# Optimization experiments

Measured on AMD Instinct MI355X. Metric: run time of the kernel, lower is better.

The kernel has to match this reference:

```python
import jax, jax.numpy as jnp
import numpy as np

B, S, D_IN, D_OUT = 2, 2048, 4096, 4096
E, K, R = 8, 2, 16
SCALING = 32.0 / 16.0  # lora_alpha / r (use_rslora=False)


def setup_inputs() -> dict:
    key = jax.random.key(0)
    ks = jax.random.split(key, 6)
    x = jax.random.normal(ks[0], (B, S, D_IN), dtype=jnp.float32)
    gate_w = jax.random.normal(ks[1], (E, D_IN), dtype=jnp.float32) * 0.02
    base_w = jax.random.normal(ks[2], (D_OUT, D_IN), dtype=jnp.float32) * 0.02
    base_b = jax.random.normal(ks[3], (D_OUT,), dtype=jnp.float32) * 0.02
    lora_A = jax.random.normal(ks[4], (E, R, D_IN), dtype=jnp.float32) * 0.02
    lora_B = jax.random.normal(ks[5], (E, D_OUT, R), dtype=jnp.float32) * 0.02
    return {"x": x, "gate_w": gate_w, "base_w": base_w, "base_b": base_b,
            "lora_A": lora_A, "lora_B": lora_B}


def reference(x, gate_w, base_w, base_b, lora_A, lora_B):
    # gate + top-k routing
    gate_logits = jnp.einsum('bsd,ed->bse', x, gate_w)           # [B,S,E]
    weights, selected = jax.lax.top_k(gate_logits, K)            # [B,S,K]
    weights = jax.nn.softmax(weights.astype(jnp.float32), axis=2).astype(x.dtype)
    # base linear
    result = jnp.einsum('bsd,od->bso', x, base_w) + base_b       # [B,S,O]
    # scatter routing weights into a dense per-expert weight map [B,S,E]
    w_full = jnp.sum(jax.nn.one_hot(selected, E, dtype=x.dtype) * weights[..., None], axis=2)
    # low-rank LoRA for every expert (tiny r), combine weighted per token
    low = jnp.einsum('bsd,erd->ebsr', x, lora_A)                 # [E,B,S,R]
    lora_out = jnp.einsum('ebsr,eor,bse->bso', low, lora_B, w_full)
    result = result + SCALING * lora_out
    return result
```

## Files before the change

kernel.cpp:

```cpp
#include <hip/hip_runtime.h>
#include <hip/hip_bf16.h>

typedef unsigned short u16;
typedef __bf16  bf16x8 __attribute__((ext_vector_type(8)));
typedef float   f32x4  __attribute__((ext_vector_type(4)));

#define T_TOK 4096
#define DIN   4096
#define DOUT  4096
#define NEXP  8
#define ER    128
#define SPLIT 8
#define KCH   (DIN / SPLIT)

#define OFF_XB    0u
#define OFF_WB    33554432u
#define OFF_AB    67108864u
#define OFF_BS2   68157440u
#define OFF_U     69206016u
#define OFF_BBF   70254592u
#define OFF_LG    70270976u
#define OFF_GPART 70402048u

__device__ __forceinline__ void async16(void* lds, const void* g) {
    __builtin_amdgcn_global_load_lds(
        (const __attribute__((address_space(1))) void*)g,
        (__attribute__((address_space(3))) void*)lds,
        16, 0, 0);
}

static __device__ __forceinline__ u16 f2b(float f) {
    __hip_bfloat16 h = __float2bfloat16(f);
    return *(u16*)&h;
}

__device__ __forceinline__ bf16x8 lds8(const u16* base, int row, int grp) {
    return *(const bf16x8*)((const char*)base + row * 128 + (((grp ^ row) & 7) * 16));
}

__global__ __launch_bounds__(256) void convert_big(const float* __restrict__ x,
                                                   const float* __restrict__ w,
                                                   uint4* __restrict__ xb,
                                                   uint4* __restrict__ wb) {
    int gid = blockIdx.x * 256 + threadIdx.x;
    const float4* s = (const float4*)((gid < 2097152) ? x : w);
    uint4* dst      = (gid < 2097152) ? xb : wb;
    int li = gid & 2097151;
    float4 a = s[2 * li], b = s[2 * li + 1];
    uint4 o;
    o.x = (unsigned)f2b(a.x) | ((unsigned)f2b(a.y) << 16);
    o.y = (unsigned)f2b(a.z) | ((unsigned)f2b(a.w) << 16);
    o.z = (unsigned)f2b(b.x) | ((unsigned)f2b(b.y) << 16);
    o.w = (unsigned)f2b(b.z) | ((unsigned)f2b(b.w) << 16);
    dst[li] = o;
}

__global__ __launch_bounds__(256) void pack_small(const float* __restrict__ lora_A,
                                                  const float* __restrict__ lora_B,
                                                  const float* __restrict__ base_b,
                                                  u16* __restrict__ ab,
                                                  u16* __restrict__ bs2,
                                                  float* __restrict__ bbf) {
    int idx = blockIdx.x * 256 + threadIdx.x;
    if (idx < 524288) {
        ab[idx] = f2b(lora_A[idx]);
    } else if (idx < 1048576) {
        int j = idx - 524288;
        int o = j >> 7, c = j & 127, e = c >> 4, r = c & 15;
        bs2[j] = f2b(lora_B[(e * DOUT + o) * 16 + r] * 2.0f);
    } else if (idx < 1052672) {
        int j = idx - 1048576;
        bbf[j] = base_b[j];
    }
}

__global__ __launch_bounds__(256) void gate_logits(const float* __restrict__ x,
                                                   const float* __restrict__ gw,
                                                   float* __restrict__ Lg) {
    const int w = threadIdx.x >> 6, lid = threadIdx.x & 63;
    const int t0 = (blockIdx.x * 4 + w) * 4;
    float acc[4][8];
#pragma unroll
    for (int j = 0; j < 4; ++j)
#pragma unroll
        for (int e = 0; e < 8; ++e) acc[j][e] = 0.f;
    for (int i = lid; i < DIN / 4; i += 64) {
        float4 gv[8];
#pragma unroll
        for (int e = 0; e < 8; ++e)
            gv[e] = ((const float4*)(gw + (size_t)e * DIN))[i];
#pragma unroll
        for (int j = 0; j < 4; ++j) {
            float4 xv = ((const float4*)(x + (size_t)(t0 + j) * DIN))[i];
#pragma unroll
            for (int e = 0; e < 8; ++e)
                acc[j][e] += xv.x * gv[e].x + xv.y * gv[e].y + xv.z * gv[e].z + xv.w * gv[e].w;
        }
    }
#pragma unroll
    for (int j = 0; j < 4; ++j)
#pragma unroll
        for (int e = 0; e < 8; ++e) {
            float v = acc[j][e];
            for (int off = 32; off; off >>= 1) v += __shfl_down(v, off, 64);
            if (lid == 0) Lg[(t0 + j) * 8 + e] = v;
        }
}

__global__ __launch_bounds__(256) void gemm1(const u16* __restrict__ X,
                                             const u16* __restrict__ ab,
                                             float* __restrict__ Gpart) {
    __shared__ __align__(16) u16 As[128 * 64];
    __shared__ __align__(16) u16 Bs[128 * 64];
    const int mb = blockIdx.x, s = blockIdx.y;
    const int w = threadIdx.x >> 6, lid = threadIdx.x & 63;
    const int lrow = lid >> 3;
    const int lcolb = ((lid & 7) ^ lrow) * 16;

    f32x4 acc[2][8];
#pragma unroll
    for (int i = 0; i < 2; ++i)
#pragma unroll
        for (int j = 0; j < 8; ++j) acc[i][j] = (f32x4){0.f, 0.f, 0.f, 0.f};

    int k0 = s * KCH;
    for (int kt = 0; kt < KCH / 64; ++kt, k0 += 64) {
#pragma unroll
        for (int q = 0; q < 4; ++q) {
            int c = w * 4 + q;
            int arow = mb * 128 + c * 8 + lrow;
            async16((char*)As + c * 1024,
                    (const char*)X + ((size_t)arow * DIN + k0) * 2 + lcolb);
            async16((char*)Bs + c * 1024,
                    (const char*)ab + ((size_t)(c * 8 + lrow) * DIN + k0) * 2 + lcolb);
        }
        __syncthreads();
        const int quad = lid >> 4, half = lid & 15;
#pragma unroll
        for (int ks8 = 0; ks8 < 8; ks8 += 4) {
            bf16x8 a[2], b[8];
#pragma unroll
            for (int i = 0; i < 2; ++i)
                a[i] = lds8(As, w * 32 + i * 16 + half, ks8 + quad);
#pragma unroll
            for (int j = 0; j < 8; ++j)
                b[j] = lds8(Bs, j * 16 + half, ks8 + quad);
#pragma unroll
            for (int i = 0; i < 2; ++i)
#pragma unroll
                for (int j = 0; j < 8; ++j)
                    acc[i][j] = __builtin_amdgcn_mfma_f32_16x16x32_bf16(a[i], b[j], acc[i][j], 0, 0, 0);
        }
        __syncthreads();
    }
    const int quad = lid >> 4, nl = lid & 15;
#pragma unroll
    for (int i = 0; i < 2; ++i)
#pragma unroll
        for (int j = 0; j < 8; ++j) {
            int n = j * 16 + nl;
            int t = mb * 128 + w * 32 + i * 16 + quad * 4;
            float* dst = Gpart + ((size_t)s * T_TOK + t) * ER + n;
#pragma unroll
            for (int r = 0; r < 4; ++r) dst[(size_t)r * ER] = acc[i][j][r];
        }
}

__global__ __launch_bounds__(256) void route_u(const float* __restrict__ Gpart,
                                               const float* __restrict__ Lg,
                                               u16* __restrict__ U) {
    __shared__ float wmap[16][9];
    const int t0 = blockIdx.x * 16;
    const int tid = threadIdx.x;
    if (tid < 16) {
        float l[8];
#pragma unroll
        for (int e = 0; e < 8; ++e) l[e] = Lg[(t0 + tid) * 8 + e];
        int e1 = 0; float b1 = l[0];
#pragma unroll
        for (int e = 1; e < 8; ++e) if (l[e] > b1) { b1 = l[e]; e1 = e; }
        int e2 = -1; float b2 = -3.4e38f;
#pragma unroll
        for (int e = 0; e < 8; ++e) if (e != e1 && l[e] > b2) { b2 = l[e]; e2 = e; }
        float ex = __expf(b2 - b1);
        float inv = 1.f / (1.f + ex);
#pragma unroll
        for (int e = 0; e < 8; ++e) wmap[tid][e] = 0.f;
        wmap[tid][e1] = inv;
        wmap[tid][e2] = ex * inv;
    }
    __syncthreads();
#pragma unroll
    for (int it = 0; it < 2; ++it) {
        int idx = it * 256 + tid;
        int tl = idx >> 5, c4 = idx & 31;
        float4 s = {0.f, 0.f, 0.f, 0.f};
        for (int sp = 0; sp < SPLIT; ++sp) {
            float4 g = ((const float4*)(Gpart + ((size_t)sp * T_TOK + t0 + tl) * ER))[c4];
            s.x += g.x; s.y += g.y; s.z += g.z; s.w += g.w;
        }
        float wv = wmap[tl][c4 >> 2];
        ushort4 o = { f2b(s.x * wv), f2b(s.y * wv), f2b(s.z * wv), f2b(s.w * wv) };
        ((ushort4*)(U + (size_t)(t0 + tl) * ER))[c4] = o;
    }
}

__global__ __launch_bounds__(256) void gemm2(const u16* __restrict__ X,
                                             const u16* __restrict__ W,
                                             const float* __restrict__ bbf,
                                             const u16* __restrict__ U,
                                             const u16* __restrict__ Bs2,
                                             float* __restrict__ out) {
    __shared__ __align__(16) u16 As[128 * 64];
    __shared__ __align__(16) u16 Bs[128 * 64];
    const int nb = blockIdx.x, mb = blockIdx.y;
    const int w = threadIdx.x >> 6, lid = threadIdx.x & 63;
    const int lrow = lid >> 3;
    const int lcolb = ((lid & 7) ^ lrow) * 16;

    f32x4 acc[4][4];
#pragma unroll
    for (int i = 0; i < 4; ++i)
#pragma unroll
        for (int j = 0; j < 4; ++j) acc[i][j] = (f32x4){0.f, 0.f, 0.f, 0.f};

    const char* pa[4]; const char* pb[4];
#pragma unroll
    for (int q = 0; q < 4; ++q) {
        int c = w * 4 + q;
        pa[q] = (const char*)X + (size_t)(mb * 128 + c * 8 + lrow) * (DIN * 2) + lcolb;
        pb[q] = (const char*)W + (size_t)(nb * 128 + c * 8 + lrow) * (DIN * 2) + lcolb;
    }

    const int quad = lid >> 4, half = lid & 15;
    const int wm = w & 1, wn = w >> 1;

#define MFMA_TILE                                                              \
    _Pragma("unroll")                                                          \
    for (int ks8 = 0; ks8 < 8; ks8 += 4) {                                     \
        bf16x8 a[4], b[4];                                                     \
        _Pragma("unroll")                                                      \
        for (int i = 0; i < 4; ++i)                                            \
            a[i] = lds8(As, wm * 64 + i * 16 + half, ks8 + quad);              \
        _Pragma("unroll")                                                      \
        for (int j = 0; j < 4; ++j)                                            \
            b[j] = lds8(Bs, wn * 64 + j * 16 + half, ks8 + quad);              \
        _Pragma("unroll")                                                      \
        for (int i = 0; i < 4; ++i)                                            \
            _Pragma("unroll")                                                  \
            for (int j = 0; j < 4; ++j)                                        \
                acc[i][j] = __builtin_amdgcn_mfma_f32_16x16x32_bf16(           \
                    a[i], b[j], acc[i][j], 0, 0, 0);                           \
    }

    for (int kt = 0; kt < 64; ++kt) {
#pragma unroll
        for (int q = 0; q < 4; ++q) {
            int c = w * 4 + q;
            async16((char*)As + c * 1024, pa[q]);
            async16((char*)Bs + c * 1024, pb[q]);
            pa[q] += 128;
            pb[q] += 128;
        }
        __syncthreads();
        MFMA_TILE
        __syncthreads();
    }
    for (int kt = 0; kt < 2; ++kt) {
#pragma unroll
        for (int q = 0; q < 4; ++q) {
            int c = w * 4 + q;
            async16((char*)As + c * 1024,
                    (const char*)U + (size_t)(mb * 128 + c * 8 + lrow) * (ER * 2) + kt * 128 + lcolb);
            async16((char*)Bs + c * 1024,
                    (const char*)Bs2 + (size_t)(nb * 128 + c * 8 + lrow) * (ER * 2) + kt * 128 + lcolb);
        }
        __syncthreads();
        MFMA_TILE
        __syncthreads();
    }

    const int nl = lid & 15;
#pragma unroll
    for (int j = 0; j < 4; ++j) {
        int n = nb * 128 + wn * 64 + j * 16 + nl;
        float bz = bbf[n];
#pragma unroll
        for (int i = 0; i < 4; ++i) {
            int m = mb * 128 + wm * 64 + i * 16 + quad * 4;
            float* dst = out + (size_t)m * DOUT + n;
#pragma unroll
            for (int r = 0; r < 4; ++r)
                dst[(size_t)r * DOUT] = acc[i][j][r] + bz;
        }
    }
}

extern "C" void kernel_launch(void* const* d_in, const int* in_sizes, int n_in,
                              void* d_out, int out_size, void* d_ws, size_t ws_size,
                              hipStream_t stream) {
    const float* x      = (const float*)d_in[0];
    const float* gate_w = (const float*)d_in[1];
    const float* base_w = (const float*)d_in[2];
    const float* base_b = (const float*)d_in[3];
    const float* lora_A = (const float*)d_in[4];
    const float* lora_B = (const float*)d_in[5];
    float* out = (float*)d_out;

    char* ws = (char*)d_ws;
    u16*   xb    = (u16*)(ws + OFF_XB);
    u16*   wb    = (u16*)(ws + OFF_WB);
    u16*   ab    = (u16*)(ws + OFF_AB);
    u16*   bs2   = (u16*)(ws + OFF_BS2);
    u16*   U     = (u16*)(ws + OFF_U);
    float* bbf   = (float*)(ws + OFF_BBF);
    float* Lg    = (float*)(ws + OFF_LG);
    float* Gpart = (float*)(ws + OFF_GPART);

    convert_big<<<16384, 256, 0, stream>>>(x, base_w, (uint4*)xb, (uint4*)wb);
    pack_small<<<4112, 256, 0, stream>>>(lora_A, lora_B, base_b, ab, bs2, bbf);
    gate_logits<<<T_TOK / 16, 256, 0, stream>>>(x, gate_w, Lg);
    gemm1<<<dim3(32, SPLIT), 256, 0, stream>>>(xb, ab, Gpart);
    route_u<<<T_TOK / 16, 256, 0, stream>>>(Gpart, Lg, U);
    gemm2<<<dim3(32, 32), 256, 0, stream>>>(xb, wb, bbf, U, bs2, out);
}
```

Before: 363.5 us.

## Rewrite base GEMM with 256x256 tiles, double-buffered async LDS pipeline

The main GEMM moves from 128x128 tiles with 4 waves to 256x256 tiles with 8 waves. It double-buffers async global-to-LDS loads with explicit vmcnt waits and raw barriers, and adds a swizzled block order and MFMA priority hints. The aim is to overlap memory loads with MFMA work and raise operand reuse per tile. The cost is 128KB of dynamic LDS, one block per CU, a 256-block grid on a GPU with more CUs than that, and hand-tuned waitcnt logic that is fragile.

```diff
diff --git a/kernel.cpp b/kernel.cpp
--- a/kernel.cpp
+++ b/kernel.cpp
@@ -37,6 +37,13 @@
 __device__ __forceinline__ bf16x8 lds8(const u16* base, int row, int grp) {
     return *(const bf16x8*)((const char*)base + row * 128 + (((grp ^ row) & 7) * 16));
 }
+
+#define FENCE() asm volatile("" ::: "memory")
+#define RAW_BAR() do { FENCE(); __builtin_amdgcn_s_barrier(); FENCE(); } while (0)
+#define LGKM0() do { asm volatile("s_waitcnt lgkmcnt(0)" ::: "memory"); \
+                     __builtin_amdgcn_sched_barrier(0); } while (0)
+#define WAITV(N) do { asm volatile("s_waitcnt vmcnt(" #N ")" ::: "memory"); \
+                      __builtin_amdgcn_sched_barrier(0); } while (0)
 
 __global__ __launch_bounds__(256) void convert_big(const float* __restrict__ x,
                                                    const float* __restrict__ w,
@@ -205,89 +212,114 @@
     }
 }
 
-__global__ __launch_bounds__(256) void gemm2(const u16* __restrict__ X,
+__global__ __launch_bounds__(512) void gemm2(const u16* __restrict__ X,
                                              const u16* __restrict__ W,
                                              const float* __restrict__ bbf,
                                              const u16* __restrict__ U,
                                              const u16* __restrict__ Bs2,
                                              float* __restrict__ out) {
-    __shared__ __align__(16) u16 As[128 * 64];
-    __shared__ __align__(16) u16 Bs[128 * 64];
-    const int nb = blockIdx.x, mb = blockIdx.y;
-    const int w = threadIdx.x >> 6, lid = threadIdx.x & 63;
-    const int lrow = lid >> 3;
-    const int lcolb = ((lid & 7) ^ lrow) * 16;
-
-    f32x4 acc[4][4];
-#pragma unroll
-    for (int i = 0; i < 4; ++i)
+    extern __shared__ __align__(16) char smem[];
+    const int tid = threadIdx.x;
+    const int l = tid & 63, w = tid >> 6;
+    const int wm = w & 1, wn = w >> 1;
+
+    const int bid = blockIdx.x;
+    const int sw = (bid & 7) * 32 + (bid >> 3);
+    const int mb = sw >> 4, nb = sw & 15;
+
+    const int srow = w * 16 + (l >> 2);
+    const int gcol = (((l & 3) ^ ((l >> 3) & 3)) << 3);
+    const int ldso = w * 1024;
+
+    const int hl = l & 15;
+    const int sgr = (((l >> 4) ^ ((hl >> 1) & 3)) << 4);
+    const int rbA = (wm * 128 + hl) * 64 + sgr;
+    const int rbB = (wn * 64 + hl) * 64 + sgr;
+
+    const u16* xrow = X   + (size_t)(mb * 256 + srow) * DIN;
+    const u16* wrw  = W   + (size_t)(nb * 256 + srow) * DIN;
+    const u16* urow = U   + (size_t)(mb * 256 + srow) * ER;
+    const u16* brow = Bs2 + (size_t)(nb * 256 + srow) * ER;
+
+    f32x4 acc[8][4];
+#pragma unroll
+    for (int i = 0; i < 8; ++i)
 #pragma unroll
         for (int j = 0; j < 4; ++j) acc[i][j] = (f32x4){0.f, 0.f, 0.f, 0.f};
 
-    const char* pa[4]; const char* pb[4];
-#pragma unroll
-    for (int q = 0; q < 4; ++q) {
-        int c = w * 4 + q;
-        pa[q] = (const char*)X + (size_t)(mb * 128 + c * 8 + lrow) * (DIN * 2) + lcolb;
-        pb[q] = (const char*)W + (size_t)(nb * 128 + c * 8 + lrow) * (DIN * 2) + lcolb;
-    }
-
-    const int quad = lid >> 4, half = lid & 15;
-    const int wm = w & 1, wn = w >> 1;
-
-#define MFMA_TILE                                                              \
-    _Pragma("unroll")                                                          \
-    for (int ks8 = 0; ks8 < 8; ks8 += 4) {                                     \
-        bf16x8 a[4], b[4];                                                     \
-        _Pragma("unroll")                                                      \
-        for (int i = 0; i < 4; ++i)                                            \
-            a[i] = lds8(As, wm * 64 + i * 16 + half, ks8 + quad);              \
-        _Pragma("unroll")                                                      \
-        for (int j = 0; j < 4; ++j)                                            \
-            b[j] = lds8(Bs, wn * 64 + j * 16 + half, ks8 + quad);              \
-        _Pragma("unroll")                                                      \
-        for (int i = 0; i < 4; ++i)                                            \
-            _Pragma("unroll")                                                  \
-            for (int j = 0; j < 4; ++j)                                        \
-                acc[i][j] = __builtin_amdgcn_mfma_f32_16x16x32_bf16(           \
-                    a[i], b[j], acc[i][j], 0, 0, 0);                           \
-    }
-
-    for (int kt = 0; kt < 64; ++kt) {
-#pragma unroll
-        for (int q = 0; q < 4; ++q) {
-            int c = w * 4 + q;
-            async16((char*)As + c * 1024, pa[q]);
-            async16((char*)Bs + c * 1024, pb[q]);
-            pa[q] += 128;
-            pb[q] += 128;
-        }
-        __syncthreads();
-        MFMA_TILE
-        __syncthreads();
-    }
-    for (int kt = 0; kt < 2; ++kt) {
-#pragma unroll
-        for (int q = 0; q < 4; ++q) {
-            int c = w * 4 + q;
-            async16((char*)As + c * 1024,
-                    (const char*)U + (size_t)(mb * 128 + c * 8 + lrow) * (ER * 2) + kt * 128 + lcolb);
-            async16((char*)Bs + c * 1024,
-                    (const char*)Bs2 + (size_t)(nb * 128 + c * 8 + lrow) * (ER * 2) + kt * 128 + lcolb);
-        }
-        __syncthreads();
-        MFMA_TILE
-        __syncthreads();
-    }
-
-    const int nl = lid & 15;
+    auto stage = [&](int c, int ks, int t2) {
+        char* dst = smem + (c << 16) + (ks << 14) + ldso;
+        if (t2 < 64) {
+            const int col = t2 * 64 + ks * 32 + gcol;
+            async16(dst,         xrow + col);
+            async16(dst + 8192,  xrow + (size_t)128 * DIN + col);
+            async16(dst + 32768, wrw + col);
+            async16(dst + 40960, wrw + (size_t)128 * DIN + col);
+        } else {
+            const int col = (t2 - 64) * 64 + ks * 32 + gcol;
+            async16(dst,         urow + col);
+            async16(dst + 8192,  urow + 128 * ER + col);
+            async16(dst + 32768, brow + col);
+            async16(dst + 40960, brow + 128 * ER + col);
+        }
+    };
+
+    stage(0, 0, 0); stage(0, 1, 0);
+    stage(1, 0, 1); stage(1, 1, 1);
+    WAITV(8);
+    RAW_BAR();
+
+#pragma unroll 2
+    for (int t = 0; t < 66; ++t) {
+        const int c = t & 1;
+        const char* seg = smem + (c << 16);
+        {
+            bf16x8 a[8], b[4];
+#pragma unroll
+            for (int i = 0; i < 8; ++i) a[i] = *(const bf16x8*)(seg + rbA + i * 1024);
+#pragma unroll
+            for (int j = 0; j < 4; ++j) b[j] = *(const bf16x8*)(seg + 32768 + rbB + j * 1024);
+            LGKM0();
+            RAW_BAR();
+            if (t + 2 < 66) stage(c, 0, t + 2);
+            __builtin_amdgcn_s_setprio(1);
+#pragma unroll
+            for (int i = 0; i < 8; ++i)
+#pragma unroll
+                for (int j = 0; j < 4; ++j)
+                    acc[i][j] = __builtin_amdgcn_mfma_f32_16x16x32_bf16(a[i], b[j], acc[i][j], 0, 0, 0);
+            __builtin_amdgcn_s_setprio(0);
+        }
+        {
+            const char* seg1 = seg + 16384;
+            bf16x8 a[8], b[4];
+#pragma unroll
+            for (int i = 0; i < 8; ++i) a[i] = *(const bf16x8*)(seg1 + rbA + i * 1024);
+#pragma unroll
+            for (int j = 0; j < 4; ++j) b[j] = *(const bf16x8*)(seg1 + 32768 + rbB + j * 1024);
+            LGKM0();
+            RAW_BAR();
+            if (t + 2 < 66) stage(c, 1, t + 2);
+            if (t < 64) { WAITV(8); } else { WAITV(0); }
+            RAW_BAR();
+            __builtin_amdgcn_s_setprio(1);
+#pragma unroll
+            for (int i = 0; i < 8; ++i)
+#pragma unroll
+                for (int j = 0; j < 4; ++j)
+                    acc[i][j] = __builtin_amdgcn_mfma_f32_16x16x32_bf16(a[i], b[j], acc[i][j], 0, 0, 0);
+            __builtin_amdgcn_s_setprio(0);
+        }
+    }
+
+    const int quad = l >> 4;
 #pragma unroll
     for (int j = 0; j < 4; ++j) {
-        int n = nb * 128 + wn * 64 + j * 16 + nl;
-        float bz = bbf[n];
-#pragma unroll
-        for (int i = 0; i < 4; ++i) {
-            int m = mb * 128 + wm * 64 + i * 16 + quad * 4;
+        const int n = nb * 256 + wn * 64 + j * 16 + hl;
+        const float bz = bbf[n];
+#pragma unroll
+        for (int i = 0; i < 8; ++i) {
+            const int m = mb * 256 + wm * 128 + i * 16 + quad * 4;
             float* dst = out + (size_t)m * DOUT + n;
 #pragma unroll
             for (int r = 0; r < 4; ++r)
@@ -317,10 +349,17 @@
     float* Lg    = (float*)(ws + OFF_LG);
     float* Gpart = (float*)(ws + OFF_GPART);
 
+    static bool attr_done = false;
+    if (!attr_done) {
+        (void)hipFuncSetAttribute(reinterpret_cast<const void*>(gemm2),
+                                  hipFuncAttributeMaxDynamicSharedMemorySize, 131072);
+        attr_done = true;
+    }
+
     convert_big<<<16384, 256, 0, stream>>>(x, base_w, (uint4*)xb, (uint4*)wb);
     pack_small<<<4112, 256, 0, stream>>>(lora_A, lora_B, base_b, ab, bs2, bbf);
     gate_logits<<<T_TOK / 16, 256, 0, stream>>>(x, gate_w, Lg);
     gemm1<<<dim3(32, SPLIT), 256, 0, stream>>>(xb, ab, Gpart);
     route_u<<<T_TOK / 16, 256, 0, stream>>>(Gpart, Lg, U);
-    gemm2<<<dim3(32, 32), 256, 0, stream>>>(xb, wb, bbf, U, bs2, out);
-}
+    gemm2<<<256, 512, 131072, stream>>>(xb, wb, bbf, U, bs2, out);
+}
```

Result: slower. 535.1 us (+47.2%).
